# Optimization experiments

Measured on AMD Instinct MI355X. Metric: run time of the kernel, lower is better.

Reference implementation:

```python
import jax, jax.numpy as jnp
import numpy as np

NUM_HEAD = 16
D = 1024
HEAD_DIM = D // NUM_HEAD
EPS = 1e-5


def setup_inputs() -> dict:
    key = jax.random.key(0)
    ks = jax.random.split(key, 7)
    B, S = 2, 2048
    s = 1.0 / np.sqrt(D)
    return {
        "x": jax.random.normal(ks[0], (B, S, D), dtype=jnp.float32),
        "wq": jax.random.uniform(ks[1], (D, D), jnp.float32, -s, s),
        "bq": jax.random.uniform(ks[2], (D,), jnp.float32, -s, s),
        "wk": jax.random.uniform(ks[3], (D, D), jnp.float32, -s, s),
        "bk": jax.random.uniform(ks[4], (D,), jnp.float32, -s, s),
        "wv": jax.random.uniform(ks[5], (D, D), jnp.float32, -s, s),
        "bv": jax.random.uniform(ks[6], (D,), jnp.float32, -s, s),
        "gamma": jnp.ones((D,), jnp.float32),
        "beta": jnp.zeros((D,), jnp.float32),
    }


def reference(x, wq, bq, wk, bk, wv, bv, gamma, beta):
    B, S, Dm = x.shape
    # Linear: x @ W^T + b (torch convention), then split heads -> [B, H, S, hd]
    def proj(w, b):
        y = jnp.einsum("bsd,ed->bse", x, w) + b
        return y.reshape(B, S, NUM_HEAD, HEAD_DIM).transpose(0, 2, 1, 3)

    q = proj(wq, bq)
    k = proj(wk, bk)
    v = proj(wv, bv)

    scores = jnp.einsum("bhqd,bhkd->bhqk", q, k) / np.sqrt(HEAD_DIM).astype(x.dtype)
    attn = jax.nn.softmax(scores, axis=-1)
    out = jnp.einsum("bhqk,bhkd->bhqd", attn, v)
    out = out.transpose(0, 2, 1, 3).reshape(B, S, Dm)

    out = out + x
    mu = jnp.mean(out, axis=-1, keepdims=True)
    var = jnp.var(out, axis=-1, keepdims=True)
    out = (out - mu) * jax.lax.rsqrt(var + EPS) * gamma + beta
    return out
```

## Files before the change

### kernel.cpp

```cpp
#include <hip/hip_runtime.h>

typedef unsigned short u16;
typedef unsigned int   u32;
typedef __bf16 bf16x8 __attribute__((ext_vector_type(8)));
typedef float  f32x4  __attribute__((ext_vector_type(4)));

#define D_MODEL 1024
#define SEQ     2048
#define NHEAD   16
#define HD      64
#define SOFTMAX_SCL 0.18033688011112042f

__device__ __forceinline__ u16 f2bf(float f) {
    u32 u;
    __builtin_memcpy(&u, &f, 4);
    u32 r = (u + 0x7fffu + ((u >> 16) & 1u)) >> 16;
    return (u16)r;
}

__device__ __forceinline__ void async_copy16(const u16* g, u16* l) {
    __builtin_amdgcn_global_load_lds(
        (__attribute__((address_space(1))) void*)g,
        (__attribute__((address_space(3))) void*)l, 16, 0, 0);
}

#define NX4 ((2 * SEQ * D_MODEL) / 4)
#define NW4 ((D_MODEL * D_MODEL) / 4)
__global__ __launch_bounds__(256) void conv_all(
    const float* __restrict__ x,  const float* __restrict__ wq,
    const float* __restrict__ wk, const float* __restrict__ wv,
    u16* __restrict__ xb, u16* __restrict__ wqb,
    u16* __restrict__ wkb, u16* __restrict__ wvb)
{
    int i = blockIdx.x * 256 + threadIdx.x;
    const float* src; u16* dst; int off;
    if (i < NX4)            { src = x;  dst = xb;  off = i; }
    else if (i < NX4 + NW4) { src = wq; dst = wqb; off = i - NX4; }
    else if (i < NX4 + 2 * NW4) { src = wk; dst = wkb; off = i - NX4 - NW4; }
    else                    { src = wv; dst = wvb; off = i - NX4 - 2 * NW4; }
    float4 a = ((const float4*)src)[off];
    ushort4 o;
    o.x = f2bf(a.x); o.y = f2bf(a.y); o.z = f2bf(a.z); o.w = f2bf(a.w);
    ((ushort4*)dst)[off] = o;
}

__global__ __launch_bounds__(256) void qkv_gemm(
    const u16* __restrict__ xb,
    const u16* __restrict__ wqb, const float* __restrict__ bq,
    const u16* __restrict__ wkb, const float* __restrict__ bk,
    const u16* __restrict__ wvb, const float* __restrict__ bv,
    u16* __restrict__ qb, u16* __restrict__ kb, u16* __restrict__ vt)
{
    const int z = blockIdx.z;
    const u16* Ap; const u16* Bp;
    int m0, n0;
    if (z < 2) {
        Ap = xb; Bp = (z == 1) ? wkb : wqb;
        m0 = blockIdx.y * 128;
        n0 = blockIdx.x * 128;
    } else {
        Ap = wvb; Bp = xb;
        m0 = blockIdx.x * 128;
        n0 = blockIdx.y * 128;
    }

    __shared__ u16 As[128 * 64];
    __shared__ u16 Bs[128 * 64];

    const int tid  = threadIdx.x;
    const int wave = tid >> 6;
    const int lane = tid & 63;
    const int quad = lane >> 4;
    const int l16  = lane & 15;
    const int wm   = wave >> 1;
    const int wn   = wave & 1;
    const int swz  = l16 & 7;

    int rr[4], co[4];
#pragma unroll
    for (int t = 0; t < 4; ++t) {
        int ch = (wave * 4 + t) * 64 + lane;
        rr[t] = ch >> 3;
        co[t] = ((ch & 7) ^ (rr[t] & 7)) * 8;
    }

    f32x4 acc[4][4] = {};

    for (int kt = 0; kt < D_MODEL; kt += 64) {
        __syncthreads();
#pragma unroll
        for (int t = 0; t < 4; ++t) {
            int chbase = (wave * 4 + t) * 64;
            async_copy16(Ap + (size_t)(m0 + rr[t]) * D_MODEL + kt + co[t], As + chbase * 8);
            async_copy16(Bp + (size_t)(n0 + rr[t]) * D_MODEL + kt + co[t], Bs + chbase * 8);
        }
        __syncthreads();

#pragma unroll
        for (int kc = 0; kc < 2; ++kc) {
            bf16x8 af[4], bf_[4];
#pragma unroll
            for (int i = 0; i < 4; ++i)
                af[i] = *(const bf16x8*)&As[(wm * 64 + i * 16 + l16) * 64 + (((kc * 4 + quad) ^ swz) << 3)];
#pragma unroll
            for (int j = 0; j < 4; ++j)
                bf_[j] = *(const bf16x8*)&Bs[(wn * 64 + j * 16 + l16) * 64 + (((kc * 4 + quad) ^ swz) << 3)];
#pragma unroll
            for (int i = 0; i < 4; ++i)
#pragma unroll
                for (int j = 0; j < 4; ++j)
                    acc[i][j] = __builtin_amdgcn_mfma_f32_16x16x32_bf16(af[i], bf_[j], acc[i][j], 0, 0, 0);
        }
    }

    if (z < 2) {
        u16* out = (z == 1) ? kb : qb;
        const float* bi = (z == 1) ? bk : bq;
        const float scl = (z == 1) ? 1.0f : SOFTMAX_SCL;
#pragma unroll
        for (int j = 0; j < 4; ++j) {
            int col = n0 + wn * 64 + j * 16 + l16;
            float bias = bi[col];
            int colbase = col & ~63;
            int dc  = (col >> 3) & 7;
            int dlo = col & 7;
#pragma unroll
            for (int i = 0; i < 4; ++i) {
#pragma unroll
                for (int r = 0; r < 4; ++r) {
                    int row = m0 + wm * 64 + i * 16 + quad * 4 + r;
                    size_t addr = (size_t)row * D_MODEL + colbase + ((dc ^ (row & 7)) << 3) + dlo;
                    out[addr] = f2bf((acc[i][j][r] + bias) * scl);
                }
            }
        }
    } else {
#pragma unroll
        for (int i = 0; i < 4; ++i) {
#pragma unroll
            for (int r = 0; r < 4; ++r) {
                int feat = m0 + wm * 64 + i * 16 + quad * 4 + r;
                float bias = bv[feat];
                int h = feat >> 6, d = feat & 63;
#pragma unroll
                for (int j = 0; j < 4; ++j) {
                    int tok = n0 + wn * 64 + j * 16 + l16;
                    int b = tok >> 11, s = tok & 2047;
                    size_t addr = ((size_t)(b * NHEAD + h) * HD + d) * SEQ
                                + (s & ~63) + (((((s >> 3) & 7) ^ (d & 7)) << 3)) + (s & 7);
                    vt[addr] = f2bf(acc[i][j][r] + bias);
                }
            }
        }
    }
}

__global__ __launch_bounds__(256) void attn_kernel(
    const u16* __restrict__ qb, const u16* __restrict__ kb, const u16* __restrict__ vtg,
    float* __restrict__ ob)
{
    const int bid = blockIdx.x;
    const int bh  = bid & 31;
    const int b   = bh >> 4;
    const int h   = bh & 15;
    const int q0  = (bid >> 5) * 128;

    const int tid  = threadIdx.x;
    const int wave = tid >> 6;
    const int lane = tid & 63;
    const int quad = lane >> 4;
    const int l16  = lane & 15;
    const int swz  = l16 & 7;

    __shared__ u16 KsB[2][4096];
    __shared__ u16 VtB[2][4096];
    __shared__ u16 Ps[8 * 1024];

    const size_t kbase = (size_t)b * SEQ * D_MODEL + h * 64;
    const size_t vbase = (size_t)(b * NHEAD + h) * HD * SEQ;

    bf16x8 aq[2][2];
#pragma unroll
    for (int rb = 0; rb < 2; ++rb) {
        const int qrow = q0 + wave * 32 + rb * 16 + l16;
        const u16* qrp = qb + (size_t)qrow * D_MODEL + h * 64;
        aq[rb][0] = *(const bf16x8*)(qrp + ((quad ^ swz) << 3));
        aq[rb][1] = *(const bf16x8*)(qrp + (((4 + quad) ^ swz) << 3));
    }

    const int r0 = tid >> 3, r1 = (tid + 256) >> 3;
    const int cs8 = (tid & 7) * 8;
    const u16* kg0 = kb + kbase + (size_t)r0 * D_MODEL + cs8;
    const u16* kg1 = kb + kbase + (size_t)r1 * D_MODEL + cs8;
    const u16* vg0 = vtg + vbase + (size_t)r0 * SEQ + cs8;
    const u16* vg1 = vtg + vbase + (size_t)r1 * SEQ + cs8;
    const int wofs = wave * 512;

    f32x4 oacc[2][4] = {};
    float lsum[2][4] = {};

    async_copy16(kg0, &KsB[0][wofs]);
    async_copy16(kg1, &KsB[0][2048 + wofs]);
    async_copy16(vg0, &VtB[0][wofs]);
    async_copy16(vg1, &VtB[0][2048 + wofs]);
    kg0 += 64 * D_MODEL; kg1 += 64 * D_MODEL;
    vg0 += 64;           vg1 += 64;

    for (int t = 0; t < SEQ / 64; ++t) {
        __syncthreads();
        if (t < SEQ / 64 - 1) {
            const int nb_ = (t + 1) & 1;
            async_copy16(kg0, &KsB[nb_][wofs]);
            async_copy16(kg1, &KsB[nb_][2048 + wofs]);
            async_copy16(vg0, &VtB[nb_][wofs]);
            async_copy16(vg1, &VtB[nb_][2048 + wofs]);
            kg0 += 64 * D_MODEL; kg1 += 64 * D_MODEL;
            vg0 += 64;           vg1 += 64;
        }
        const u16* Ks = KsB[t & 1];
        const u16* Vt = VtB[t & 1];

        f32x4 sacc[2][4] = {};
#pragma unroll
        for (int c = 0; c < 2; ++c) {
            bf16x8 bk_[4];
#pragma unroll
            for (int nb = 0; nb < 4; ++nb)
                bk_[nb] = *(const bf16x8*)&Ks[(nb * 16 + l16) * 64 + (((c * 4 + quad) ^ swz) << 3)];
#pragma unroll
            for (int rb = 0; rb < 2; ++rb)
#pragma unroll
                for (int nb = 0; nb < 4; ++nb)
                    sacc[rb][nb] = __builtin_amdgcn_mfma_f32_16x16x32_bf16(aq[rb][c], bk_[nb], sacc[rb][nb], 0, 0, 0);
        }

#pragma unroll
        for (int rb = 0; rb < 2; ++rb)
#pragma unroll
            for (int r = 0; r < 4; ++r)
#pragma unroll
                for (int nb = 0; nb < 4; ++nb) {
                    float e = exp2f(sacc[rb][nb][r]);
                    lsum[rb][r] += e;
                    u32 bits;
                    __builtin_memcpy(&bits, &e, 4);
                    Ps[wave * 2048 + rb * 1024 + r * 256 + nb * 64 + lane] = (u16)(bits >> 16);
                }

#pragma unroll
        for (int c = 0; c < 2; ++c) {
            bf16x8 ap[2];
#pragma unroll
            for (int rb = 0; rb < 2; ++rb)
                ap[rb] = *(const bf16x8*)&Ps[wave * 2048 + rb * 1024 + (l16 & 3) * 256
                                             + (c * 2 + (quad >> 1)) * 64
                                             + (l16 >> 2) * 16 + (quad & 1) * 8];
            bf16x8 bv_[4];
#pragma unroll
            for (int nb = 0; nb < 4; ++nb)
                bv_[nb] = *(const bf16x8*)&Vt[(nb * 16 + l16) * 64 + (((c * 4 + quad) ^ swz) << 3)];
#pragma unroll
            for (int rb = 0; rb < 2; ++rb)
#pragma unroll
                for (int nb = 0; nb < 4; ++nb)
                    oacc[rb][nb] = __builtin_amdgcn_mfma_f32_16x16x32_bf16(ap[rb], bv_[nb], oacc[rb][nb], 0, 0, 0);
        }
    }

#pragma unroll
    for (int rb = 0; rb < 2; ++rb)
#pragma unroll
        for (int r = 0; r < 4; ++r) {
            float s = lsum[rb][r];
            s += __shfl_xor(s, 1, 64);
            s += __shfl_xor(s, 2, 64);
            s += __shfl_xor(s, 4, 64);
            s += __shfl_xor(s, 8, 64);
            float inv = 1.0f / s;
            int row = q0 + wave * 32 + rb * 16 + quad * 4 + r;
#pragma unroll
            for (int nb = 0; nb < 4; ++nb) {
                int d = nb * 16 + l16;
                ob[((size_t)b * SEQ + row) * D_MODEL + h * 64 + d] = oacc[rb][nb][r] * inv;
            }
        }
}

__global__ __launch_bounds__(256) void add_ln(
    const float* __restrict__ attn, const float* __restrict__ x,
    const float* __restrict__ gamma, const float* __restrict__ beta,
    float* __restrict__ out)
{
    const int row = blockIdx.x;
    const int tid = threadIdx.x;
    const size_t rb = (size_t)row * D_MODEL;

    float4 a  = ((const float4*)(attn + rb))[tid];
    float4 xb = ((const float4*)(x + rb))[tid];

    float v[4];
    v[0] = a.x + xb.x;
    v[1] = a.y + xb.y;
    v[2] = a.z + xb.z;
    v[3] = a.w + xb.w;

    float s  = v[0] + v[1] + v[2] + v[3];
    float s2 = v[0]*v[0] + v[1]*v[1] + v[2]*v[2] + v[3]*v[3];
#pragma unroll
    for (int off = 1; off < 64; off <<= 1) {
        s  += __shfl_xor(s, off, 64);
        s2 += __shfl_xor(s2, off, 64);
    }

    __shared__ float red[2][4];
    int wave = tid >> 6, lane = tid & 63;
    if (lane == 0) { red[0][wave] = s; red[1][wave] = s2; }
    __syncthreads();
    float st  = red[0][0] + red[0][1] + red[0][2] + red[0][3];
    float s2t = red[1][0] + red[1][1] + red[1][2] + red[1][3];

    float mu   = st * (1.0f / D_MODEL);
    float var  = s2t * (1.0f / D_MODEL) - mu * mu;
    float rstd = rsqrtf(var + 1e-5f);

    float4 g  = ((const float4*)(gamma))[tid];
    float4 bt = ((const float4*)(beta))[tid];
    float4 o;
    o.x = (v[0] - mu) * rstd * g.x + bt.x;
    o.y = (v[1] - mu) * rstd * g.y + bt.y;
    o.z = (v[2] - mu) * rstd * g.z + bt.z;
    o.w = (v[3] - mu) * rstd * g.w + bt.w;
    ((float4*)(out + rb))[tid] = o;
}

extern "C" void kernel_launch(void* const* d_in, const int* in_sizes, int n_in,
                              void* d_out, int out_size, void* d_ws, size_t ws_size,
                              hipStream_t stream) {
    const float* x     = (const float*)d_in[0];
    const float* wq    = (const float*)d_in[1];
    const float* bq    = (const float*)d_in[2];
    const float* wk    = (const float*)d_in[3];
    const float* bk    = (const float*)d_in[4];
    const float* wv    = (const float*)d_in[5];
    const float* bv    = (const float*)d_in[6];
    const float* gamma = (const float*)d_in[7];
    const float* beta  = (const float*)d_in[8];
    float* outp = (float*)d_out;

    char* ws = (char*)d_ws;
    u16*   xb  = (u16*)(ws);
    u16*   wqb = (u16*)(ws + ((size_t)8  << 20));
    u16*   wkb = (u16*)(ws + ((size_t)10 << 20));
    u16*   wvb = (u16*)(ws + ((size_t)12 << 20));
    u16*   qb  = (u16*)(ws + ((size_t)16 << 20));
    u16*   kb  = (u16*)(ws + ((size_t)24 << 20));
    u16*   vt  = (u16*)(ws + ((size_t)32 << 20));
    float* ab  = (float*)(ws + ((size_t)40 << 20));

    conv_all<<<dim3((NX4 + 3 * NW4) / 256), 256, 0, stream>>>(
        x, wq, wk, wv, xb, wqb, wkb, wvb);
    qkv_gemm<<<dim3(8, 32, 3), 256, 0, stream>>>(xb, wqb, bq, wkb, bk, wvb, bv, qb, kb, vt);
    attn_kernel<<<dim3(512), 256, 0, stream>>>(qb, kb, vt, ab);
    add_ln<<<dim3(2 * SEQ), 256, 0, stream>>>(ab, x, gamma, beta, outp);
}
```

Before: 208.9 us.

## Split attention waves over query and key halves, reorder QKV GEMM block mapping

The attention kernel now arranges its 4 waves as 2 query groups × 2 key halves. Each wave handles 64 query rows against 32 keys per tile, and the two key halves are merged at the end through LDS, both the partial outputs and the row sums. K/V double buffering is dropped in favour of a single buffer loaded between two barriers each iteration, which shrinks LDS use but exposes load latency. The QKV GEMM grid is flattened to 1D with the Q/K/V/column tiles interleaved, so consecutive blocks share the same input rows and should get better cache reuse.

New measurement: 246.4 us. 1.18x slower.

```diff
diff --git a/kernel.cpp b/kernel.cpp
--- a/kernel.cpp
+++ b/kernel.cpp
@@ -51,17 +51,22 @@
     const u16* __restrict__ wvb, const float* __restrict__ bv,
     u16* __restrict__ qb, u16* __restrict__ kb, u16* __restrict__ vt)
 {
-    const int z = blockIdx.z;
+    const int bid  = blockIdx.x;
+    const int pair = bid % 24;
+    const int by   = bid / 24;
+    const int z    = pair >> 3;
+    const int bx   = pair & 7;
+
     const u16* Ap; const u16* Bp;
     int m0, n0;
     if (z < 2) {
         Ap = xb; Bp = (z == 1) ? wkb : wqb;
-        m0 = blockIdx.y * 128;
-        n0 = blockIdx.x * 128;
+        m0 = by * 128;
+        n0 = bx * 128;
     } else {
         Ap = wvb; Bp = xb;
-        m0 = blockIdx.x * 128;
-        n0 = blockIdx.y * 128;
+        m0 = bx * 128;
+        n0 = by * 128;
     }
 
     __shared__ u16 As[128 * 64];
@@ -171,21 +176,26 @@
     const int quad = lane >> 4;
     const int l16  = lane & 15;
     const int swz  = l16 & 7;
-
-    __shared__ u16 KsB[2][4096];
-    __shared__ u16 VtB[2][4096];
-    __shared__ u16 Ps[8 * 1024];
+    const int wq2  = wave >> 1;
+    const int wk2  = wave & 1;
+
+    __shared__ u16 sh[16384];
+    u16* Ks = sh;
+    u16* Vt = sh + 4096;
+    u16* Ps = sh + 8192;
+    float* OLds = (float*)sh;
+    __shared__ float lsum_lds[2][2][64];
 
     const size_t kbase = (size_t)b * SEQ * D_MODEL + h * 64;
     const size_t vbase = (size_t)(b * NHEAD + h) * HD * SEQ;
 
-    bf16x8 aq[2][2];
-#pragma unroll
-    for (int rb = 0; rb < 2; ++rb) {
-        const int qrow = q0 + wave * 32 + rb * 16 + l16;
+    bf16x8 aq[4][2];
+#pragma unroll
+    for (int g = 0; g < 4; ++g) {
+        const int qrow = q0 + wq2 * 64 + g * 16 + l16;
         const u16* qrp = qb + (size_t)qrow * D_MODEL + h * 64;
-        aq[rb][0] = *(const bf16x8*)(qrp + ((quad ^ swz) << 3));
-        aq[rb][1] = *(const bf16x8*)(qrp + (((4 + quad) ^ swz) << 3));
+        aq[g][0] = *(const bf16x8*)(qrp + ((quad ^ swz) << 3));
+        aq[g][1] = *(const bf16x8*)(qrp + (((4 + quad) ^ swz) << 3));
     }
 
     const int r0 = tid >> 3, r1 = (tid + 256) >> 3;
@@ -196,94 +206,105 @@
     const u16* vg1 = vtg + vbase + (size_t)r1 * SEQ + cs8;
     const int wofs = wave * 512;
 
-    f32x4 oacc[2][4] = {};
-    float lsum[2][4] = {};
-
-    async_copy16(kg0, &KsB[0][wofs]);
-    async_copy16(kg1, &KsB[0][2048 + wofs]);
-    async_copy16(vg0, &VtB[0][wofs]);
-    async_copy16(vg1, &VtB[0][2048 + wofs]);
-    kg0 += 64 * D_MODEL; kg1 += 64 * D_MODEL;
-    vg0 += 64;           vg1 += 64;
+    f32x4 oacc[4][4] = {};
+    float lsum[4][4] = {};
 
     for (int t = 0; t < SEQ / 64; ++t) {
         __syncthreads();
-        if (t < SEQ / 64 - 1) {
-            const int nb_ = (t + 1) & 1;
-            async_copy16(kg0, &KsB[nb_][wofs]);
-            async_copy16(kg1, &KsB[nb_][2048 + wofs]);
-            async_copy16(vg0, &VtB[nb_][wofs]);
-            async_copy16(vg1, &VtB[nb_][2048 + wofs]);
-            kg0 += 64 * D_MODEL; kg1 += 64 * D_MODEL;
-            vg0 += 64;           vg1 += 64;
-        }
-        const u16* Ks = KsB[t & 1];
-        const u16* Vt = VtB[t & 1];
-
-        f32x4 sacc[2][4] = {};
-#pragma unroll
-        for (int c = 0; c < 2; ++c) {
-            bf16x8 bk_[4];
-#pragma unroll
-            for (int nb = 0; nb < 4; ++nb)
-                bk_[nb] = *(const bf16x8*)&Ks[(nb * 16 + l16) * 64 + (((c * 4 + quad) ^ swz) << 3)];
-#pragma unroll
-            for (int rb = 0; rb < 2; ++rb)
-#pragma unroll
-                for (int nb = 0; nb < 4; ++nb)
-                    sacc[rb][nb] = __builtin_amdgcn_mfma_f32_16x16x32_bf16(aq[rb][c], bk_[nb], sacc[rb][nb], 0, 0, 0);
-        }
-
-#pragma unroll
-        for (int rb = 0; rb < 2; ++rb)
-#pragma unroll
-            for (int r = 0; r < 4; ++r)
-#pragma unroll
-                for (int nb = 0; nb < 4; ++nb) {
-                    float e = exp2f(sacc[rb][nb][r]);
-                    lsum[rb][r] += e;
+        async_copy16(kg0, Ks + wofs);
+        async_copy16(kg1, Ks + 2048 + wofs);
+        async_copy16(vg0, Vt + wofs);
+        async_copy16(vg1, Vt + 2048 + wofs);
+        kg0 += 64 * D_MODEL; kg1 += 64 * D_MODEL;
+        vg0 += 64;           vg1 += 64;
+        __syncthreads();
+
+        bf16x8 kf[2][2];
+#pragma unroll
+        for (int kb2 = 0; kb2 < 2; ++kb2)
+#pragma unroll
+            for (int c = 0; c < 2; ++c)
+                kf[kb2][c] = *(const bf16x8*)&Ks[(wk2 * 32 + kb2 * 16 + l16) * 64
+                                                 + (((c * 4 + quad) ^ swz) << 3)];
+
+        f32x4 sacc[4][2] = {};
+#pragma unroll
+        for (int g = 0; g < 4; ++g)
+#pragma unroll
+            for (int kb2 = 0; kb2 < 2; ++kb2) {
+                sacc[g][kb2] = __builtin_amdgcn_mfma_f32_16x16x32_bf16(aq[g][0], kf[kb2][0], sacc[g][kb2], 0, 0, 0);
+                sacc[g][kb2] = __builtin_amdgcn_mfma_f32_16x16x32_bf16(aq[g][1], kf[kb2][1], sacc[g][kb2], 0, 0, 0);
+            }
+
+#pragma unroll
+        for (int g = 0; g < 4; ++g)
+#pragma unroll
+            for (int kb2 = 0; kb2 < 2; ++kb2)
+#pragma unroll
+                for (int r = 0; r < 4; ++r) {
+                    float e = exp2f(sacc[g][kb2][r]);
+                    lsum[g][r] += e;
                     u32 bits;
                     __builtin_memcpy(&bits, &e, 4);
-                    Ps[wave * 2048 + rb * 1024 + r * 256 + nb * 64 + lane] = (u16)(bits >> 16);
+                    Ps[wave * 2048 + (g * 16 + quad * 4 + r) * 32 + kb2 * 16 + l16] = (u16)(bits >> 16);
                 }
 
-#pragma unroll
-        for (int c = 0; c < 2; ++c) {
-            bf16x8 ap[2];
-#pragma unroll
-            for (int rb = 0; rb < 2; ++rb)
-                ap[rb] = *(const bf16x8*)&Ps[wave * 2048 + rb * 1024 + (l16 & 3) * 256
-                                             + (c * 2 + (quad >> 1)) * 64
-                                             + (l16 >> 2) * 16 + (quad & 1) * 8];
-            bf16x8 bv_[4];
+        bf16x8 vf[4];
+#pragma unroll
+        for (int nb = 0; nb < 4; ++nb)
+            vf[nb] = *(const bf16x8*)&Vt[(nb * 16 + l16) * 64 + (((wk2 * 4 + quad) ^ swz) << 3)];
+
+#pragma unroll
+        for (int g = 0; g < 4; ++g) {
+            bf16x8 ap = *(const bf16x8*)&Ps[wave * 2048 + (g * 16 + l16) * 32 + quad * 8];
 #pragma unroll
             for (int nb = 0; nb < 4; ++nb)
-                bv_[nb] = *(const bf16x8*)&Vt[(nb * 16 + l16) * 64 + (((c * 4 + quad) ^ swz) << 3)];
-#pragma unroll
-            for (int rb = 0; rb < 2; ++rb)
-#pragma unroll
-                for (int nb = 0; nb < 4; ++nb)
-                    oacc[rb][nb] = __builtin_amdgcn_mfma_f32_16x16x32_bf16(ap[rb], bv_[nb], oacc[rb][nb], 0, 0, 0);
-        }
-    }
-
-#pragma unroll
-    for (int rb = 0; rb < 2; ++rb)
+                oacc[g][nb] = __builtin_amdgcn_mfma_f32_16x16x32_bf16(ap, vf[nb], oacc[g][nb], 0, 0, 0);
+        }
+    }
+
+#pragma unroll
+    for (int g = 0; g < 4; ++g)
 #pragma unroll
         for (int r = 0; r < 4; ++r) {
-            float s = lsum[rb][r];
+            float s = lsum[g][r];
             s += __shfl_xor(s, 1, 64);
             s += __shfl_xor(s, 2, 64);
             s += __shfl_xor(s, 4, 64);
             s += __shfl_xor(s, 8, 64);
-            float inv = 1.0f / s;
-            int row = q0 + wave * 32 + rb * 16 + quad * 4 + r;
-#pragma unroll
-            for (int nb = 0; nb < 4; ++nb) {
-                int d = nb * 16 + l16;
-                ob[((size_t)b * SEQ + row) * D_MODEL + h * 64 + d] = oacc[rb][nb][r] * inv;
+            lsum[g][r] = s;
+            if (l16 == 0) lsum_lds[wq2][wk2][g * 16 + quad * 4 + r] = s;
+        }
+    __syncthreads();
+
+    if (wk2 == 1) {
+#pragma unroll
+        for (int g = 0; g < 4; ++g)
+#pragma unroll
+            for (int nb = 0; nb < 4; ++nb)
+#pragma unroll
+                for (int r = 0; r < 4; ++r)
+                    OLds[(size_t)wq2 * 4096 + (g * 16 + quad * 4 + r) * 64 + nb * 16 + l16]
+                        = oacc[g][nb][r];
+    }
+    __syncthreads();
+
+    if (wk2 == 0) {
+#pragma unroll
+        for (int g = 0; g < 4; ++g)
+#pragma unroll
+            for (int r = 0; r < 4; ++r) {
+                int qr = g * 16 + quad * 4 + r;
+                float inv = 1.0f / (lsum[g][r] + lsum_lds[wq2][1][qr]);
+                int row = q0 + wq2 * 64 + qr;
+#pragma unroll
+                for (int nb = 0; nb < 4; ++nb) {
+                    int d = nb * 16 + l16;
+                    float o = oacc[g][nb][r] + OLds[(size_t)wq2 * 4096 + qr * 64 + nb * 16 + l16];
+                    ob[((size_t)b * SEQ + row) * D_MODEL + h * 64 + d] = o * inv;
+                }
             }
-        }
+    }
 }
 
 __global__ __launch_bounds__(256) void add_ln(
@@ -359,7 +380,7 @@
 
     conv_all<<<dim3((NX4 + 3 * NW4) / 256), 256, 0, stream>>>(
         x, wq, wk, wv, xb, wqb, wkb, wvb);
-    qkv_gemm<<<dim3(8, 32, 3), 256, 0, stream>>>(xb, wqb, bq, wkb, bk, wvb, bv, qb, kb, vt);
+    qkv_gemm<<<dim3(24 * 32), 256, 0, stream>>>(xb, wqb, bq, wkb, bk, wvb, bv, qb, kb, vt);
     attn_kernel<<<dim3(512), 256, 0, stream>>>(qb, kb, vt, ab);
     add_ln<<<dim3(2 * SEQ), 256, 0, stream>>>(ab, x, gamma, beta, outp);
 }
```

## Split attention over two KV halves and merge partials in the add+LayerNorm kernel

Applied to the files above, without the earlier changes.

The attention kernel now launches twice as many blocks, each covering half of the key sequence. Each block writes unnormalized bf16 partial outputs plus per-row exp-sums, and add_ln sums the two partials, divides by the combined sum and then applies the residual and LayerNorm. The aim is more parallelism and occupancy in attention, and a halved byte size for the intermediate written to and read from global memory. In exchange, the K/V double-buffered prefetch is replaced by a single buffer with two barriers per tile, partials are rounded to bf16, and the QKV GEMM grid is flattened to 1D to change block ordering.

Result: faster. 202.8 us (-2.9%).

```diff
diff --git a/kernel.cpp b/kernel.cpp
--- a/kernel.cpp
+++ b/kernel.cpp
@@ -16,6 +16,12 @@
     __builtin_memcpy(&u, &f, 4);
     u32 r = (u + 0x7fffu + ((u >> 16) & 1u)) >> 16;
     return (u16)r;
+}
+__device__ __forceinline__ float bf2f(u16 v) {
+    u32 u = ((u32)v) << 16;
+    float f;
+    __builtin_memcpy(&f, &u, 4);
+    return f;
 }
 
 __device__ __forceinline__ void async_copy16(const u16* g, u16* l) {
@@ -51,17 +57,22 @@
     const u16* __restrict__ wvb, const float* __restrict__ bv,
     u16* __restrict__ qb, u16* __restrict__ kb, u16* __restrict__ vt)
 {
-    const int z = blockIdx.z;
+    const int bid  = blockIdx.x;
+    const int pair = bid % 24;
+    const int by   = bid / 24;
+    const int z    = pair >> 3;
+    const int bx   = pair & 7;
+
     const u16* Ap; const u16* Bp;
     int m0, n0;
     if (z < 2) {
         Ap = xb; Bp = (z == 1) ? wkb : wqb;
-        m0 = blockIdx.y * 128;
-        n0 = blockIdx.x * 128;
+        m0 = by * 128;
+        n0 = bx * 128;
     } else {
         Ap = wvb; Bp = xb;
-        m0 = blockIdx.x * 128;
-        n0 = blockIdx.y * 128;
+        m0 = bx * 128;
+        n0 = by * 128;
     }
 
     __shared__ u16 As[128 * 64];
@@ -157,13 +168,14 @@
 
 __global__ __launch_bounds__(256) void attn_kernel(
     const u16* __restrict__ qb, const u16* __restrict__ kb, const u16* __restrict__ vtg,
-    float* __restrict__ ob)
+    u16* __restrict__ abp, float* __restrict__ lsums)
 {
-    const int bid = blockIdx.x;
-    const int bh  = bid & 31;
-    const int b   = bh >> 4;
-    const int h   = bh & 15;
-    const int q0  = (bid >> 5) * 128;
+    const int bid  = blockIdx.x;
+    const int bh   = bid & 31;
+    const int b    = bh >> 4;
+    const int h    = bh & 15;
+    const int q0   = ((bid >> 5) & 15) * 128;
+    const int half = bid >> 9;
 
     const int tid  = threadIdx.x;
     const int wave = tid >> 6;
@@ -172,8 +184,8 @@
     const int l16  = lane & 15;
     const int swz  = l16 & 7;
 
-    __shared__ u16 KsB[2][4096];
-    __shared__ u16 VtB[2][4096];
+    __shared__ u16 Ks[4096];
+    __shared__ u16 Vt[4096];
     __shared__ u16 Ps[8 * 1024];
 
     const size_t kbase = (size_t)b * SEQ * D_MODEL + h * 64;
@@ -190,35 +202,24 @@
 
     const int r0 = tid >> 3, r1 = (tid + 256) >> 3;
     const int cs8 = (tid & 7) * 8;
-    const u16* kg0 = kb + kbase + (size_t)r0 * D_MODEL + cs8;
-    const u16* kg1 = kb + kbase + (size_t)r1 * D_MODEL + cs8;
-    const u16* vg0 = vtg + vbase + (size_t)r0 * SEQ + cs8;
-    const u16* vg1 = vtg + vbase + (size_t)r1 * SEQ + cs8;
+    const u16* kg0 = kb + kbase + (size_t)(half * 1024 + r0) * D_MODEL + cs8;
+    const u16* kg1 = kb + kbase + (size_t)(half * 1024 + r1) * D_MODEL + cs8;
+    const u16* vg0 = vtg + vbase + (size_t)r0 * SEQ + half * 1024 + cs8;
+    const u16* vg1 = vtg + vbase + (size_t)r1 * SEQ + half * 1024 + cs8;
     const int wofs = wave * 512;
 
     f32x4 oacc[2][4] = {};
     float lsum[2][4] = {};
 
-    async_copy16(kg0, &KsB[0][wofs]);
-    async_copy16(kg1, &KsB[0][2048 + wofs]);
-    async_copy16(vg0, &VtB[0][wofs]);
-    async_copy16(vg1, &VtB[0][2048 + wofs]);
-    kg0 += 64 * D_MODEL; kg1 += 64 * D_MODEL;
-    vg0 += 64;           vg1 += 64;
-
-    for (int t = 0; t < SEQ / 64; ++t) {
+    for (int t = 0; t < 16; ++t) {
         __syncthreads();
-        if (t < SEQ / 64 - 1) {
-            const int nb_ = (t + 1) & 1;
-            async_copy16(kg0, &KsB[nb_][wofs]);
-            async_copy16(kg1, &KsB[nb_][2048 + wofs]);
-            async_copy16(vg0, &VtB[nb_][wofs]);
-            async_copy16(vg1, &VtB[nb_][2048 + wofs]);
-            kg0 += 64 * D_MODEL; kg1 += 64 * D_MODEL;
-            vg0 += 64;           vg1 += 64;
-        }
-        const u16* Ks = KsB[t & 1];
-        const u16* Vt = VtB[t & 1];
+        async_copy16(kg0, Ks + wofs);
+        async_copy16(kg1, Ks + 2048 + wofs);
+        async_copy16(vg0, Vt + wofs);
+        async_copy16(vg1, Vt + 2048 + wofs);
+        kg0 += 64 * D_MODEL; kg1 += 64 * D_MODEL;
+        vg0 += 64;           vg1 += 64;
+        __syncthreads();
 
         f32x4 sacc[2][4] = {};
 #pragma unroll
@@ -276,45 +277,55 @@
             s += __shfl_xor(s, 2, 64);
             s += __shfl_xor(s, 4, 64);
             s += __shfl_xor(s, 8, 64);
-            float inv = 1.0f / s;
             int row = q0 + wave * 32 + rb * 16 + quad * 4 + r;
+            if (l16 == 0)
+                lsums[((size_t)bh * 2 + half) * SEQ + row] = s;
 #pragma unroll
             for (int nb = 0; nb < 4; ++nb) {
                 int d = nb * 16 + l16;
-                ob[((size_t)b * SEQ + row) * D_MODEL + h * 64 + d] = oacc[rb][nb][r] * inv;
+                abp[(size_t)half * SEQ * 2 * D_MODEL
+                    + ((size_t)b * SEQ + row) * D_MODEL + h * 64 + d] = f2bf(oacc[rb][nb][r]);
             }
         }
 }
 
 __global__ __launch_bounds__(256) void add_ln(
-    const float* __restrict__ attn, const float* __restrict__ x,
+    const u16* __restrict__ abp, const float* __restrict__ lsums,
+    const float* __restrict__ x,
     const float* __restrict__ gamma, const float* __restrict__ beta,
     float* __restrict__ out)
 {
     const int row = blockIdx.x;
     const int tid = threadIdx.x;
     const size_t rb = (size_t)row * D_MODEL;
-
-    float4 a  = ((const float4*)(attn + rb))[tid];
+    const int b = row >> 11, s = row & 2047;
+    const int h = tid >> 4;
+    const int bh = b * NHEAD + h;
+
+    float l = lsums[(size_t)bh * 2 * SEQ + s] + lsums[((size_t)bh * 2 + 1) * SEQ + s];
+    float inv = 1.0f / l;
+
+    uint2 a0 = ((const uint2*)(abp + rb))[tid];
+    uint2 a1 = ((const uint2*)(abp + (size_t)SEQ * 2 * D_MODEL + rb))[tid];
     float4 xb = ((const float4*)(x + rb))[tid];
 
     float v[4];
-    v[0] = a.x + xb.x;
-    v[1] = a.y + xb.y;
-    v[2] = a.z + xb.z;
-    v[3] = a.w + xb.w;
-
-    float s  = v[0] + v[1] + v[2] + v[3];
+    v[0] = (bf2f((u16)(a0.x & 0xffff)) + bf2f((u16)(a1.x & 0xffff))) * inv + xb.x;
+    v[1] = (bf2f((u16)(a0.x >> 16))    + bf2f((u16)(a1.x >> 16)))    * inv + xb.y;
+    v[2] = (bf2f((u16)(a0.y & 0xffff)) + bf2f((u16)(a1.y & 0xffff))) * inv + xb.z;
+    v[3] = (bf2f((u16)(a0.y >> 16))    + bf2f((u16)(a1.y >> 16)))    * inv + xb.w;
+
+    float sm  = v[0] + v[1] + v[2] + v[3];
     float s2 = v[0]*v[0] + v[1]*v[1] + v[2]*v[2] + v[3]*v[3];
 #pragma unroll
     for (int off = 1; off < 64; off <<= 1) {
-        s  += __shfl_xor(s, off, 64);
+        sm += __shfl_xor(sm, off, 64);
         s2 += __shfl_xor(s2, off, 64);
     }
 
     __shared__ float red[2][4];
     int wave = tid >> 6, lane = tid & 63;
-    if (lane == 0) { red[0][wave] = s; red[1][wave] = s2; }
+    if (lane == 0) { red[0][wave] = sm; red[1][wave] = s2; }
     __syncthreads();
     float st  = red[0][0] + red[0][1] + red[0][2] + red[0][3];
     float s2t = red[1][0] + red[1][1] + red[1][2] + red[1][3];
@@ -348,18 +359,19 @@
     float* outp = (float*)d_out;
 
     char* ws = (char*)d_ws;
-    u16*   xb  = (u16*)(ws);
-    u16*   wqb = (u16*)(ws + ((size_t)8  << 20));
-    u16*   wkb = (u16*)(ws + ((size_t)10 << 20));
-    u16*   wvb = (u16*)(ws + ((size_t)12 << 20));
-    u16*   qb  = (u16*)(ws + ((size_t)16 << 20));
-    u16*   kb  = (u16*)(ws + ((size_t)24 << 20));
-    u16*   vt  = (u16*)(ws + ((size_t)32 << 20));
-    float* ab  = (float*)(ws + ((size_t)40 << 20));
+    u16*   xb    = (u16*)(ws);
+    u16*   wqb   = (u16*)(ws + ((size_t)8  << 20));
+    u16*   wkb   = (u16*)(ws + ((size_t)10 << 20));
+    u16*   wvb   = (u16*)(ws + ((size_t)12 << 20));
+    u16*   qb    = (u16*)(ws + ((size_t)16 << 20));
+    u16*   kb    = (u16*)(ws + ((size_t)24 << 20));
+    u16*   vt    = (u16*)(ws + ((size_t)32 << 20));
+    u16*   abp   = (u16*)(ws + ((size_t)40 << 20));
+    float* lsums = (float*)(ws + ((size_t)56 << 20));
 
     conv_all<<<dim3((NX4 + 3 * NW4) / 256), 256, 0, stream>>>(
         x, wq, wk, wv, xb, wqb, wkb, wvb);
-    qkv_gemm<<<dim3(8, 32, 3), 256, 0, stream>>>(xb, wqb, bq, wkb, bk, wvb, bv, qb, kb, vt);
-    attn_kernel<<<dim3(512), 256, 0, stream>>>(qb, kb, vt, ab);
-    add_ln<<<dim3(2 * SEQ), 256, 0, stream>>>(ab, x, gamma, beta, outp);
-}
+    qkv_gemm<<<dim3(24 * 32), 256, 0, stream>>>(xb, wqb, bq, wkb, bk, wvb, bv, qb, kb, vt);
+    attn_kernel<<<dim3(1024), 256, 0, stream>>>(qb, kb, vt, abp, lsums);
+    add_ln<<<dim3(2 * SEQ), 256, 0, stream>>>(abp, lsums, x, gamma, beta, outp);
+}
```
